# Performance work log

Hardware: AMD Instinct MI355X
Metric: run time of the kernel (lower is better)

The kernel has to match this reference:

```python
import jax, jax.numpy as jnp
import numpy as np

EMBED_DIM = 1024
NUM_HEADS = 16
HEAD_DIM = EMBED_DIM // NUM_HEADS


def setup_inputs() -> dict:
    key = jax.random.key(0)
    k1, k2, k3, k4, k5 = jax.random.split(key, 5)
    B, S, D = 2, 2048, EMBED_DIM
    s_in = 1.0 / np.sqrt(D)
    x = jax.random.normal(k1, (B, S, D), dtype=jnp.float32)
    W_qkv = jax.random.uniform(k2, (D, 3 * D), dtype=jnp.float32, minval=-s_in, maxval=s_in)
    b_qkv = jax.random.uniform(k3, (3 * D,), dtype=jnp.float32, minval=-s_in, maxval=s_in)
    W_out = jax.random.uniform(k4, (D, D), dtype=jnp.float32, minval=-s_in, maxval=s_in)
    b_out = jax.random.uniform(k5, (D,), dtype=jnp.float32, minval=-s_in, maxval=s_in)
    return {"x": x, "W_qkv": W_qkv, "b_qkv": b_qkv, "W_out": W_out, "b_out": b_out}


def reference(x, W_qkv, b_qkv, W_out, b_out):
    B, S, D = x.shape
    H, Hd = NUM_HEADS, HEAD_DIM
    qkv = x @ W_qkv + b_qkv                      # [B,S,3D]
    qkv = qkv.reshape(B, S, 3, H, Hd)
    q = qkv[:, :, 0].transpose(0, 2, 1, 3)       # [B,H,S,Hd]
    k = qkv[:, :, 1].transpose(0, 2, 1, 3)
    v = qkv[:, :, 2].transpose(0, 2, 1, 3)
    scores = jnp.einsum('bhsd,bhtd->bhst', q, k) / jnp.sqrt(jnp.float32(Hd))
    attn = jax.nn.softmax(scores, axis=-1)       # dropout is identity in eval mode
    out = jnp.einsum('bhst,bhtd->bhsd', attn, v)
    out = out.transpose(0, 2, 1, 3).reshape(B, S, D)
    return out @ W_out + b_out
```

## Files before the change

kernel.cpp:

```cpp
#include <hip/hip_runtime.h>
#include <stdint.h>
#include <math.h>

#define EMBED 1024
#define HEADS 16
#define HDIM  64
#define SEQ   2048
#define BATCH 2

typedef __bf16 bf16x8 __attribute__((ext_vector_type(8)));
typedef float  f32x4  __attribute__((ext_vector_type(4)));
typedef unsigned short u16x8 __attribute__((ext_vector_type(8)));
typedef unsigned short u16x4 __attribute__((ext_vector_type(4)));

static __device__ __forceinline__ unsigned short f2bf(float f){
  union { float f; uint32_t u; } v; v.f = f;
  uint32_t u = v.u;
  uint32_t r = (u + 0x7FFFu + ((u >> 16) & 1u)) >> 16;
  return (unsigned short)r;
}
static __device__ __forceinline__ bf16x8 as_bf(u16x8 v){ return __builtin_bit_cast(bf16x8, v); }

static __device__ __forceinline__ uint32_t pk_bf16(float a, float b){
#if defined(__has_builtin) && __has_builtin(__builtin_amdgcn_cvt_pk_bf16_f32)
  typedef __bf16 bf16x2 __attribute__((ext_vector_type(2)));
  bf16x2 p = __builtin_amdgcn_cvt_pk_bf16_f32(a, b);
  return __builtin_bit_cast(uint32_t, p);
#else
  return (uint32_t)f2bf(a) | ((uint32_t)f2bf(b) << 16);
#endif
}

static __device__ __forceinline__ float fexp2(float x){
#if defined(__has_builtin) && __has_builtin(__builtin_amdgcn_exp2f)
  return __builtin_amdgcn_exp2f(x);
#else
  return exp2f(x);
#endif
}

static __device__ __forceinline__ void stage16(const unsigned short* gp,
                                               unsigned short* lp_wave, int lane){
#if defined(__has_builtin) && __has_builtin(__builtin_amdgcn_global_load_lds)
  __builtin_amdgcn_global_load_lds((const __attribute__((address_space(1))) void*)gp,
                                   (__attribute__((address_space(3))) void*)lp_wave,
                                   16, 0, 0);
#else
  *(u16x8*)(lp_wave + lane * 8) = *(const u16x8*)gp;
#endif
}

__global__ __launch_bounds__(256) void cast_x(const float* __restrict__ in,
                                              unsigned short* __restrict__ out){
  int i = (blockIdx.x * 256 + threadIdx.x) * 4;
  float4 v = *(const float4*)(in + i);
  u16x4 o;
  o[0] = f2bf(v.x); o[1] = f2bf(v.y); o[2] = f2bf(v.z); o[3] = f2bf(v.w);
  *(u16x4*)(out + i) = o;
}

__global__ __launch_bounds__(256) void wtrans(const float* __restrict__ W,
                                              unsigned short* __restrict__ Wt,
                                              int N, int K){
  __shared__ unsigned short T[32 * 36];
  int t = threadIdx.x;
  int n0 = blockIdx.x * 32, k0 = blockIdx.y * 32;
  int kr = t >> 3, nc = (t & 7) * 4;
  float4 wv = *(const float4*)(W + (size_t)(k0 + kr) * N + n0 + nc);
  T[(nc + 0) * 36 + kr] = f2bf(wv.x);
  T[(nc + 1) * 36 + kr] = f2bf(wv.y);
  T[(nc + 2) * 36 + kr] = f2bf(wv.z);
  T[(nc + 3) * 36 + kr] = f2bf(wv.w);
  __syncthreads();
  int nr = t >> 3, kc = (t & 7) * 4;
  *(u16x4*)(Wt + (size_t)(n0 + nr) * K + k0 + kc) = *(const u16x4*)&T[nr * 36 + kc];
}

__global__ __launch_bounds__(256) void vtrans(const unsigned short* __restrict__ V,
                                              unsigned short* __restrict__ VT){
  __shared__ unsigned short T[32 * 36];
  int t = threadIdx.x;
  int s0 = blockIdx.x * 32, d0 = blockIdx.y * 32;
  size_t base = (size_t)blockIdx.z * SEQ * HDIM;
  int sr = t >> 3, dc = (t & 7) * 4;
  u16x4 vv = *(const u16x4*)(V + base + (size_t)(s0 + sr) * HDIM + d0 + dc);
  T[(dc + 0) * 36 + sr] = vv[0];
  T[(dc + 1) * 36 + sr] = vv[1];
  T[(dc + 2) * 36 + sr] = vv[2];
  T[(dc + 3) * 36 + sr] = vv[3];
  __syncthreads();
  int dr = t >> 3, sc = (t & 7) * 4;
  *(u16x4*)(VT + base + (size_t)(d0 + dr) * SEQ + s0 + sc) = *(const u16x4*)&T[dr * 36 + sc];
}

template<int MODE>
__global__ __launch_bounds__(256) void gemm_bf16(
    const unsigned short* __restrict__ A,
    const unsigned short* __restrict__ Bt,
    const float* __restrict__ bias,
    float* __restrict__ Cout,
    unsigned short* __restrict__ q_ws,
    unsigned short* __restrict__ k_ws,
    unsigned short* __restrict__ v_ws,
    int M, int N, int K)
{
  __shared__ unsigned short As[128 * 32];
  __shared__ unsigned short Bs[128 * 32];
  const int tid  = threadIdx.x;
  const int bm   = blockIdx.y, bn = blockIdx.x;
  const int w    = tid >> 6, lane = tid & 63;
  const int quad = lane >> 4, l16 = lane & 15;
  const int wm   = (w >> 1) * 64, wn = (w & 1) * 64;

  f32x4 acc[4][4] = {};

  for (int k0 = 0; k0 < K; k0 += 32) {
    #pragma unroll
    for (int i = 0; i < 2; i++){
      int c = w + i * 4;
      int row = c * 16 + (lane >> 2);
      int kg = (lane & 3) ^ (row & 3);
      stage16(A  + (size_t)(bm * 128 + row) * K + k0 + kg * 8, &As[c * 512], lane);
      stage16(Bt + (size_t)(bn * 128 + row) * K + k0 + kg * 8, &Bs[c * 512], lane);
    }
    __syncthreads();

    bf16x8 af[4], bfr[4];
    #pragma unroll
    for (int t = 0; t < 4; t++){
      int ra = wm + t * 16 + l16;
      int rb = wn + t * 16 + l16;
      af[t]  = as_bf(*(const u16x8*)&As[(ra << 5) + ((quad ^ (ra & 3)) << 3)]);
      bfr[t] = as_bf(*(const u16x8*)&Bs[(rb << 5) + ((quad ^ (rb & 3)) << 3)]);
    }
    #pragma unroll
    for (int mt = 0; mt < 4; mt++)
      #pragma unroll
      for (int nt = 0; nt < 4; nt++)
        acc[mt][nt] = __builtin_amdgcn_mfma_f32_16x16x32_bf16(af[mt], bfr[nt], acc[mt][nt], 0, 0, 0);
    __syncthreads();
  }

  #pragma unroll
  for (int mt = 0; mt < 4; mt++){
    #pragma unroll
    for (int nt = 0; nt < 4; nt++){
      #pragma unroll
      for (int r = 0; r < 4; r++){
        int gm = bm * 128 + wm + mt * 16 + quad * 4 + r;
        int gn = bn * 128 + wn + nt * 16 + l16;
        float val = acc[mt][nt][r] + bias[gn];
        if (MODE == 0){
          int which = gn >> 10, rem = gn & 1023;
          int h = rem >> 6, hd = rem & 63;
          int b = gm >> 11, s = gm & 2047;
          size_t off = ((size_t)(b * HEADS + h) * SEQ + s) * HDIM + hd;
          if (which == 0)      q_ws[off] = f2bf(val * 0.18033688f);
          else if (which == 1) k_ws[off] = f2bf(val);
          else                 v_ws[off] = f2bf(val);
        } else {
          Cout[(size_t)gm * N + gn] = val;
        }
      }
    }
  }
}

__global__ __launch_bounds__(256) void attn(
    const unsigned short* __restrict__ q_ws,
    const unsigned short* __restrict__ k_ws,
    const unsigned short* __restrict__ vt_ws,
    unsigned short* __restrict__ o_ws)
{
  __shared__ unsigned short Qs[128 * 64];
  __shared__ unsigned short Ks[64 * 64];
  __shared__ unsigned short VTs[64 * 64];
  __shared__ unsigned short Ps[4][32 * 64];
  const int tid  = threadIdx.x;
  const int qt   = blockIdx.x, bh = blockIdx.y;
  const int w    = tid >> 6, lane = tid & 63;
  const int quad = lane >> 4, l16 = lane & 15;
  const size_t base = (size_t)bh * SEQ * HDIM;

  #pragma unroll
  for (int i = 0; i < 4; i++){
    int c = w * 4 + i;
    int row = c * 8 + (lane >> 3);
    int kg = (lane & 7) ^ (row & 7);
    stage16(q_ws + base + (size_t)(qt * 128 + row) * HDIM + kg * 8, &Qs[c * 512], lane);
  }

  int srow[2], skg[2];
  #pragma unroll
  for (int i = 0; i < 2; i++){
    int c = w * 2 + i;
    srow[i] = c * 8 + (lane >> 3);
    skg[i]  = (lane & 7) ^ (srow[i] & 7);
  }

  #pragma unroll
  for (int i = 0; i < 2; i++){
    int c = w * 2 + i;
    stage16(k_ws  + base + (size_t)srow[i] * HDIM + skg[i] * 8, &Ks[c * 512],  lane);
    stage16(vt_ws + base + (size_t)srow[i] * SEQ + skg[i] * 8,  &VTs[c * 512], lane);
  }
  __syncthreads();

  f32x4 acc[2][4] = {};
  f32x4 li[2] = {};

  for (int kt = 0; kt < SEQ / 64; kt++){
    u16x8 kpre[2], vpre[2];
    if (kt < SEQ / 64 - 1){
      #pragma unroll
      for (int i = 0; i < 2; i++){
        kpre[i] = *(const u16x8*)(k_ws  + base + (size_t)((kt + 1) * 64 + srow[i]) * HDIM + skg[i] * 8);
        vpre[i] = *(const u16x8*)(vt_ws + base + (size_t)srow[i] * SEQ + (kt + 1) * 64 + skg[i] * 8);
      }
    }

    f32x4 sf[2][4] = {};
    #pragma unroll
    for (int ks = 0; ks < 2; ks++){
      bf16x8 aq[2];
      #pragma unroll
      for (int mq = 0; mq < 2; mq++){
        int row = w * 32 + mq * 16 + l16;
        aq[mq] = as_bf(*(const u16x8*)&Qs[(row << 6) + ((((ks << 2) + quad) ^ (row & 7)) << 3)]);
      }
      #pragma unroll
      for (int nt = 0; nt < 4; nt++){
        int rk = nt * 16 + l16;
        bf16x8 bk = as_bf(*(const u16x8*)&Ks[(rk << 6) + ((((ks << 2) + quad) ^ (rk & 7)) << 3)]);
        #pragma unroll
        for (int mq = 0; mq < 2; mq++)
          sf[mq][nt] = __builtin_amdgcn_mfma_f32_16x16x32_bf16(aq[mq], bk, sf[mq][nt], 0, 0, 0);
      }
    }

    #pragma unroll
    for (int mq = 0; mq < 2; mq++)
      #pragma unroll
      for (int nt = 0; nt < 4; nt++)
        #pragma unroll
        for (int r = 0; r < 4; r++)
          sf[mq][nt][r] = fexp2(sf[mq][nt][r]);
    #pragma unroll
    for (int mq = 0; mq < 2; mq++)
      #pragma unroll
      for (int r = 0; r < 4; r++)
        li[mq][r] += (sf[mq][0][r] + sf[mq][1][r]) + (sf[mq][2][r] + sf[mq][3][r]);

    #pragma unroll
    for (int mq = 0; mq < 2; mq++){
      #pragma unroll
      for (int nt = 0; nt < 4; nt++){
        #pragma unroll
        for (int r = 0; r < 4; r++){
          int prow = mq * 16 + quad * 4 + r;
          int cg = nt * 2 + (l16 >> 3);
          Ps[w][(prow << 6) + ((cg ^ (prow & 7)) << 3) + (l16 & 7)] = f2bf(sf[mq][nt][r]);
        }
      }
    }

    #pragma unroll
    for (int k2 = 0; k2 < 2; k2++){
      bf16x8 ap[2];
      #pragma unroll
      for (int mq = 0; mq < 2; mq++){
        int pr = mq * 16 + l16;
        ap[mq] = as_bf(*(const u16x8*)&Ps[w][(pr << 6) + ((((k2 << 2) + quad) ^ (pr & 7)) << 3)]);
      }
      #pragma unroll
      for (int nt = 0; nt < 4; nt++){
        int rv = nt * 16 + l16;
        bf16x8 bv = as_bf(*(const u16x8*)&VTs[(rv << 6) + ((((k2 << 2) + quad) ^ (rv & 7)) << 3)]);
        #pragma unroll
        for (int mq = 0; mq < 2; mq++)
          acc[mq][nt] = __builtin_amdgcn_mfma_f32_16x16x32_bf16(ap[mq], bv, acc[mq][nt], 0, 0, 0);
      }
    }
    __syncthreads();

    if (kt < SEQ / 64 - 1){
      #pragma unroll
      for (int i = 0; i < 2; i++){
        int c = w * 2 + i;
        *(u16x8*)&Ks[c * 512 + lane * 8]  = kpre[i];
        *(u16x8*)&VTs[c * 512 + lane * 8] = vpre[i];
      }
      __syncthreads();
    }
  }

  #pragma unroll
  for (int off = 1; off < 16; off <<= 1)
    #pragma unroll
    for (int mq = 0; mq < 2; mq++)
      #pragma unroll
      for (int r = 0; r < 4; r++)
        li[mq][r] += __shfl_xor(li[mq][r], off);

  float inv[2][4];
  #pragma unroll
  for (int mq = 0; mq < 2; mq++)
    #pragma unroll
    for (int r = 0; r < 4; r++)
      inv[mq][r] = 1.0f / li[mq][r];

  int b = bh >> 4, h = bh & 15;
  #pragma unroll
  for (int mq = 0; mq < 2; mq++)
    #pragma unroll
    for (int nt = 0; nt < 4; nt++)
      #pragma unroll
      for (int r = 0; r < 4; r++){
        int s = qt * 128 + w * 32 + mq * 16 + quad * 4 + r;
        int d = h * 64 + nt * 16 + l16;
        o_ws[((size_t)(b * SEQ + s)) * EMBED + d] = f2bf(acc[mq][nt][r] * inv[mq][r]);
      }
}

extern "C" void kernel_launch(void* const* d_in, const int* in_sizes, int n_in,
                              void* d_out, int out_size, void* d_ws, size_t ws_size,
                              hipStream_t stream) {
  const float* x     = (const float*)d_in[0];
  const float* W_qkv = (const float*)d_in[1];
  const float* b_qkv = (const float*)d_in[2];
  const float* W_out = (const float*)d_in[3];
  const float* b_out = (const float*)d_in[4];
  float* out = (float*)d_out;

  char* ws = (char*)d_ws;
  unsigned short* xb    = (unsigned short*)(ws);
  unsigned short* q     = (unsigned short*)(ws + ((size_t)8  << 20));
  unsigned short* k     = (unsigned short*)(ws + ((size_t)16 << 20));
  unsigned short* v     = (unsigned short*)(ws + ((size_t)24 << 20));
  unsigned short* vt    = (unsigned short*)(ws + ((size_t)32 << 20));
  unsigned short* wqkvT = (unsigned short*)(ws + ((size_t)32 << 20));
  unsigned short* woutT = (unsigned short*)(ws + ((size_t)24 << 20));
  unsigned short* o     = xb;

  cast_x<<<dim3(4096), dim3(256), 0, stream>>>(x, xb);

  wtrans<<<dim3(96, 32), dim3(256), 0, stream>>>(W_qkv, wqkvT, 3072, 1024);

  gemm_bf16<0><<<dim3(24, 32), dim3(256), 0, stream>>>(
      xb, wqkvT, b_qkv, nullptr, q, k, v, 4096, 3072, 1024);

  vtrans<<<dim3(64, 2, 32), dim3(256), 0, stream>>>(v, vt);

  wtrans<<<dim3(32, 32), dim3(256), 0, stream>>>(W_out, woutT, 1024, 1024);

  attn<<<dim3(16, 32), dim3(256), 0, stream>>>(q, k, vt, o);

  gemm_bf16<1><<<dim3(8, 32), dim3(256), 0, stream>>>(
      o, woutT, b_out, out, nullptr, nullptr, nullptr, 4096, 1024, 1024);
}
```

Before: 221.6 us.

## Keep softmax probabilities in registers by computing transposed scores and permuting V^T

```diff
diff --git a/kernel.cpp b/kernel.cpp
--- a/kernel.cpp
+++ b/kernel.cpp
@@ -12,6 +12,7 @@
 typedef float  f32x4  __attribute__((ext_vector_type(4)));
 typedef unsigned short u16x8 __attribute__((ext_vector_type(8)));
 typedef unsigned short u16x4 __attribute__((ext_vector_type(4)));
+typedef uint32_t u32x4v __attribute__((ext_vector_type(4)));
 
 static __device__ __forceinline__ unsigned short f2bf(float f){
   union { float f; uint32_t u; } v; v.f = f;
@@ -90,7 +91,8 @@
   T[(dc + 3) * 36 + sr] = vv[3];
   __syncthreads();
   int dr = t >> 3, sc = (t & 7) * 4;
-  *(u16x4*)(VT + base + (size_t)(d0 + dr) * SEQ + s0 + sc) = *(const u16x4*)&T[dr * 36 + sc];
+  int pos = (((sc >> 2) & 3) << 3) + (((sc >> 4) & 1) << 2);
+  *(u16x4*)(VT + base + (size_t)(d0 + dr) * SEQ + s0 + pos) = *(const u16x4*)&T[dr * 36 + sc];
 }
 
 template<int MODE>
@@ -175,7 +177,6 @@
   __shared__ unsigned short Qs[128 * 64];
   __shared__ unsigned short Ks[64 * 64];
   __shared__ unsigned short VTs[64 * 64];
-  __shared__ unsigned short Ps[4][32 * 64];
   const int tid  = threadIdx.x;
   const int qt   = blockIdx.x, bh = blockIdx.y;
   const int w    = tid >> 6, lane = tid & 63;
@@ -206,8 +207,17 @@
   }
   __syncthreads();
 
+  bf16x8 bq[2][2];
+  #pragma unroll
+  for (int mq = 0; mq < 2; mq++){
+    int row = w * 32 + mq * 16 + l16;
+    #pragma unroll
+    for (int ks = 0; ks < 2; ks++)
+      bq[mq][ks] = as_bf(*(const u16x8*)&Qs[(row << 6) + ((((ks << 2) + quad) ^ (row & 7)) << 3)]);
+  }
+
   f32x4 acc[2][4] = {};
-  f32x4 li[2] = {};
+  float li[2] = {0.f, 0.f};
 
   for (int kt = 0; kt < SEQ / 64; kt++){
     u16x8 kpre[2], vpre[2];
@@ -219,63 +229,48 @@
       }
     }
 
-    f32x4 sf[2][4] = {};
+    f32x4 sf[4][2] = {};
     #pragma unroll
     for (int ks = 0; ks < 2; ks++){
-      bf16x8 aq[2];
-      #pragma unroll
-      for (int mq = 0; mq < 2; mq++){
-        int row = w * 32 + mq * 16 + l16;
-        aq[mq] = as_bf(*(const u16x8*)&Qs[(row << 6) + ((((ks << 2) + quad) ^ (row & 7)) << 3)]);
-      }
       #pragma unroll
       for (int nt = 0; nt < 4; nt++){
         int rk = nt * 16 + l16;
-        bf16x8 bk = as_bf(*(const u16x8*)&Ks[(rk << 6) + ((((ks << 2) + quad) ^ (rk & 7)) << 3)]);
+        bf16x8 ak = as_bf(*(const u16x8*)&Ks[(rk << 6) + ((((ks << 2) + quad) ^ (rk & 7)) << 3)]);
         #pragma unroll
         for (int mq = 0; mq < 2; mq++)
-          sf[mq][nt] = __builtin_amdgcn_mfma_f32_16x16x32_bf16(aq[mq], bk, sf[mq][nt], 0, 0, 0);
-      }
-    }
-
-    #pragma unroll
-    for (int mq = 0; mq < 2; mq++)
-      #pragma unroll
-      for (int nt = 0; nt < 4; nt++)
+          sf[nt][mq] = __builtin_amdgcn_mfma_f32_16x16x32_bf16(ak, bq[mq][ks], sf[nt][mq], 0, 0, 0);
+      }
+    }
+
+    #pragma unroll
+    for (int nt = 0; nt < 4; nt++)
+      #pragma unroll
+      for (int mq = 0; mq < 2; mq++)
         #pragma unroll
         for (int r = 0; r < 4; r++)
-          sf[mq][nt][r] = fexp2(sf[mq][nt][r]);
+          sf[nt][mq][r] = fexp2(sf[nt][mq][r]);
     #pragma unroll
     for (int mq = 0; mq < 2; mq++)
       #pragma unroll
-      for (int r = 0; r < 4; r++)
-        li[mq][r] += (sf[mq][0][r] + sf[mq][1][r]) + (sf[mq][2][r] + sf[mq][3][r]);
-
-    #pragma unroll
-    for (int mq = 0; mq < 2; mq++){
-      #pragma unroll
-      for (int nt = 0; nt < 4; nt++){
-        #pragma unroll
-        for (int r = 0; r < 4; r++){
-          int prow = mq * 16 + quad * 4 + r;
-          int cg = nt * 2 + (l16 >> 3);
-          Ps[w][(prow << 6) + ((cg ^ (prow & 7)) << 3) + (l16 & 7)] = f2bf(sf[mq][nt][r]);
-        }
-      }
-    }
-
-    #pragma unroll
-    for (int k2 = 0; k2 < 2; k2++){
+      for (int nt = 0; nt < 4; nt++)
+        li[mq] += (sf[nt][mq][0] + sf[nt][mq][1]) + (sf[nt][mq][2] + sf[nt][mq][3]);
+
+    #pragma unroll
+    for (int c = 0; c < 2; c++){
       bf16x8 ap[2];
       #pragma unroll
       for (int mq = 0; mq < 2; mq++){
-        int pr = mq * 16 + l16;
-        ap[mq] = as_bf(*(const u16x8*)&Ps[w][(pr << 6) + ((((k2 << 2) + quad) ^ (pr & 7)) << 3)]);
+        u32x4v aw;
+        aw[0] = pk_bf16(sf[c * 2][mq][0],     sf[c * 2][mq][1]);
+        aw[1] = pk_bf16(sf[c * 2][mq][2],     sf[c * 2][mq][3]);
+        aw[2] = pk_bf16(sf[c * 2 + 1][mq][0], sf[c * 2 + 1][mq][1]);
+        aw[3] = pk_bf16(sf[c * 2 + 1][mq][2], sf[c * 2 + 1][mq][3]);
+        ap[mq] = __builtin_bit_cast(bf16x8, aw);
       }
       #pragma unroll
       for (int nt = 0; nt < 4; nt++){
         int rv = nt * 16 + l16;
-        bf16x8 bv = as_bf(*(const u16x8*)&VTs[(rv << 6) + ((((k2 << 2) + quad) ^ (rv & 7)) << 3)]);
+        bf16x8 bv = as_bf(*(const u16x8*)&VTs[(rv << 6) + ((((c << 2) + quad) ^ (rv & 7)) << 3)]);
         #pragma unroll
         for (int mq = 0; mq < 2; mq++)
           acc[mq][nt] = __builtin_amdgcn_mfma_f32_16x16x32_bf16(ap[mq], bv, acc[mq][nt], 0, 0, 0);
@@ -295,19 +290,17 @@
   }
 
   #pragma unroll
-  for (int off = 1; off < 16; off <<= 1)
-    #pragma unroll
-    for (int mq = 0; mq < 2; mq++)
-      #pragma unroll
-      for (int r = 0; r < 4; r++)
-        li[mq][r] += __shfl_xor(li[mq][r], off);
-
-  float inv[2][4];
+  for (int mq = 0; mq < 2; mq++){
+    li[mq] += __shfl_xor(li[mq], 16);
+    li[mq] += __shfl_xor(li[mq], 32);
+  }
+  float inv[2] = {1.0f / li[0], 1.0f / li[1]};
+  float invr[2][4];
   #pragma unroll
   for (int mq = 0; mq < 2; mq++)
     #pragma unroll
     for (int r = 0; r < 4; r++)
-      inv[mq][r] = 1.0f / li[mq][r];
+      invr[mq][r] = __shfl(inv[mq], quad * 4 + r);
 
   int b = bh >> 4, h = bh & 15;
   #pragma unroll
@@ -318,7 +311,7 @@
       for (int r = 0; r < 4; r++){
         int s = qt * 128 + w * 32 + mq * 16 + quad * 4 + r;
         int d = h * 64 + nt * 16 + l16;
-        o_ws[((size_t)(b * SEQ + s)) * EMBED + d] = f2bf(acc[mq][nt][r] * inv[mq][r]);
+        o_ws[((size_t)(b * SEQ + s)) * EMBED + d] = f2bf(acc[mq][nt][r] * invr[mq][r]);
       }
 }
 
```

New measurement: 209.3 us. -5.6%, faster.
